# Optimization experiments

Measured on AMD Instinct MI355X. Metric: run time of the kernel, lower is better.

## Reference

```python
import jax, jax.numpy as jnp
import numpy as np

K = 20  # number of unrolled recurrent steps


def setup_inputs() -> dict:
    key = jax.random.key(0)
    k_w, k_b, k0, k1, kv = jax.random.split(key, 5)
    B, d, h = 4096, 128, 256
    w = jax.random.normal(k_w, (B, d, d), dtype=jnp.float32) * 0.05
    b = jax.random.normal(k_b, (B, d), dtype=jnp.float32)
    W0 = jax.random.normal(k0, (h, 2 * d), dtype=jnp.float32) * 0.05
    W1 = jax.random.normal(k1, (h, h), dtype=jnp.float32) * 0.05
    V = jax.random.normal(kv, (d, h), dtype=jnp.float32) * 0.05
    return {"w": w, "b": b, "W0": W0, "W1": W1, "V": V}


def _cell(x, w, b, W0, W1, V):
    # gradient = w @ x - b  -> [B, d]
    grad = jnp.einsum('bij,bj->bi', w, x) - b
    h = jnp.concatenate([-grad, x], axis=-1)      # [B, 2d]
    h = jax.nn.relu(h @ W0.T)                     # [B, h0]
    h = jax.nn.relu(h @ W1.T)                     # [B, h1]
    return h @ V.T                                # [B, d]


def reference(w, b, W0, W1, V):
    x0 = jnp.zeros_like(b)

    def step(x, _):
        return _cell(x, w, b, W0, W1, V), None

    x, _ = jax.lax.scan(step, x0, None, length=K)
    return x
```

## Files before the change

### kernel.cpp

```cpp
#include <hip/hip_runtime.h>
#include <stdint.h>

#define KSTEPS 20
#define EPB 4
#define NBLOCKS 1024
#define NTHREADS 512

#define WQ_E_STRIDE 33792
#define FB_STRIDE   1056
#define WQ_OFF      0
#define HB_OFF      135168
#define H0B_OFF     137344
#define H1B_OFF     139520
#define SMEM_BYTES  141696

#define ACT_STRIDE 544

typedef short bf16x8 __attribute__((ext_vector_type(8)));
typedef float f32x4  __attribute__((ext_vector_type(4)));

static __device__ __forceinline__ uint32_t f2bf(float x) {
    union { float f; uint32_t u; } v; v.f = x;
    return (v.u + 0x7fffu + ((v.u >> 16) & 1u)) >> 16;
}
static __device__ __forceinline__ uint32_t packbf2(float a, float b) {
    uint32_t r;
    asm("v_cvt_pk_bf16_f32 %0, %1, %2" : "=v"(r) : "v"(a), "v"(b));
    return r;
}

__global__ void prep_kernel(const float* __restrict__ W0, const float* __restrict__ W1,
                            const float* __restrict__ V, uint16_t* __restrict__ out)
{
    int i = blockIdx.x * 256 + threadIdx.x;
    float v;
    if (i < 65536) {
        int c = i >> 11, rest = i & 2047, r = rest >> 3, m = rest & 7;
        v = W0[r * 256 + c * 8 + m];
    } else if (i < 131072) {
        int j = i - 65536;
        int c = j >> 11, rest = j & 2047, r = rest >> 3, m = rest & 7;
        v = W1[r * 256 + c * 8 + m];
    } else {
        int j = i - 131072;
        int c = j >> 10, rest = j & 1023, r = rest >> 3, m = rest & 7;
        v = V[r * 256 + c * 8 + m];
    }
    out[i] = (uint16_t)f2bf(v);
}

__global__
__attribute__((amdgpu_flat_work_group_size(512, 512), amdgpu_waves_per_eu(2, 2)))
void mlprnn_main(
    const float* __restrict__ w, const float* __restrict__ b,
    const uint16_t* __restrict__ wp, float* __restrict__ out)
{
    extern __shared__ char smem[];

    const int t  = threadIdx.x;
    const int e0 = blockIdx.x * EPB;

    const int l = t & 63, wv = t >> 6;
    const int row15 = l & 15;
    const int kg    = l >> 4;
    const int cm    = l & 3;
    const bool cok  = row15 < 4;
    const int mt0 = 2 * wv, mt1 = 2 * wv + 1;

    const int e_g  = wv >> 1;
    const int mh   = wv & 1;

    const bf16x8* w0v = (const bf16x8*)wp;
    const bf16x8* w1v = w0v + 32 * 256;
    const bf16x8* vv  = w1v + 32 * 256;

    bf16x8 a0w[8], a1w[8], b0w[8], b1w[8], vw[8];
    #pragma unroll
    for (int kk = 0; kk < 8; ++kk) {
        a0w[kk] = w0v[(kk * 4 + kg) * 256 + mt0 * 16 + row15];
        a1w[kk] = w0v[(kk * 4 + kg) * 256 + mt1 * 16 + row15];
        b0w[kk] = w1v[(kk * 4 + kg) * 256 + mt0 * 16 + row15];
        b1w[kk] = w1v[(kk * 4 + kg) * 256 + mt1 * 16 + row15];
        vw[kk]  = vv[(kk * 4 + kg) * 128 + wv * 16 + row15];
    }
    f32x4 bseed[4];
    #pragma unroll
    for (int mt = 0; mt < 4; ++mt)
        bseed[mt] = *(const f32x4*)(b + (size_t)(e0 + e_g) * 128 + mh * 64 + mt * 16 + kg * 4);

    {
        int e = t >> 7, feat = t & 127;
        float bv = b[(size_t)(e0 + e) * 128 + feat];
        *(uint16_t*)(smem + HB_OFF + e * ACT_STRIDE + feat * 2) = (uint16_t)f2bf(bv);
        *(uint16_t*)(smem + HB_OFF + e * ACT_STRIDE + 256 + feat * 2) = 0;
    }
    __syncthreads();

    #define STAGE_CHUNK(C) do {                                                   \
        const float4* wg_ = (const float4*)w;                                     \
        _Pragma("unroll")                                                         \
        for (int it = (C) * 8; it < (C) * 8 + 8; ++it) {                          \
            int g  = it * NTHREADS + t;                                           \
            int e  = g >> 12;                                                     \
            int gg = g & 4095;                                                    \
            int r  = gg >> 5, q = gg & 31;                                        \
            float4 f = wg_[(size_t)(e0 + e) * 4096 + gg];                         \
            uint2 pk = { packbf2(-f.x, -f.y), packbf2(-f.z, -f.w) };              \
            int kt_s = q >> 3, kg_s = (q >> 1) & 3, h = q & 1;                    \
            int fb   = (r >> 4) * 4 + kt_s;                                       \
            int byte = e * WQ_E_STRIDE + fb * FB_STRIDE                           \
                     + (kg_s * 16 + (r & 15)) * 16 + h * 8;                       \
            *(uint2*)(smem + WQ_OFF + byte) = pk;                                 \
        }                                                                         \
    } while (0)

    const char* wqA = smem + WQ_OFF + e_g * WQ_E_STRIDE + l * 16;
    const char* xB  = smem + HB_OFF + e_g * ACT_STRIDE + 256 + kg * 16;

    const char* hbB = smem + HB_OFF  + cm * ACT_STRIDE + kg * 16;
    const char* h0B = smem + H0B_OFF + cm * ACT_STRIDE + kg * 16;
    const char* h1B = smem + H1B_OFF + cm * ACT_STRIDE + kg * 16;

    bf16x8 gw0h[4], gw1h[4];

    #define PHASE_GRAD() do {                                                     \
        bf16x8 bx[4];                                                             \
        _Pragma("unroll")                                                         \
        for (int kt = 0; kt < 4; ++kt) bx[kt] = *(const bf16x8*)(xB + kt * 64);   \
        f32x4 ag0 = bseed[0], ag1 = bseed[1], ag2 = bseed[2], ag3 = bseed[3];     \
        _Pragma("unroll")                                                         \
        for (int kt = 0; kt < 4; ++kt) {                                          \
            bf16x8 a2 = *(const bf16x8*)(wqA + (((mh * 4 + 2) * 4 + kt) * FB_STRIDE)); \
            bf16x8 a3 = *(const bf16x8*)(wqA + (((mh * 4 + 3) * 4 + kt) * FB_STRIDE)); \
            ag0 = __builtin_amdgcn_mfma_f32_16x16x32_bf16(gw0h[kt], bx[kt], ag0, 0, 0, 0); \
            ag1 = __builtin_amdgcn_mfma_f32_16x16x32_bf16(gw1h[kt], bx[kt], ag1, 0, 0, 0); \
            ag2 = __builtin_amdgcn_mfma_f32_16x16x32_bf16(a2, bx[kt], ag2, 0, 0, 0); \
            ag3 = __builtin_amdgcn_mfma_f32_16x16x32_bf16(a3, bx[kt], ag3, 0, 0, 0); \
        }                                                                         \
        char* gw = smem + HB_OFF + e_g * ACT_STRIDE;                              \
        if (row15 == 0) *(uint2*)(gw + (mh * 64 + 0 * 16 + kg * 4) * 2)           \
            = (uint2){ packbf2(ag0[0], ag0[1]), packbf2(ag0[2], ag0[3]) };        \
        if (row15 == 1) *(uint2*)(gw + (mh * 64 + 1 * 16 + kg * 4) * 2)           \
            = (uint2){ packbf2(ag1[0], ag1[1]), packbf2(ag1[2], ag1[3]) };        \
        if (row15 == 2) *(uint2*)(gw + (mh * 64 + 2 * 16 + kg * 4) * 2)           \
            = (uint2){ packbf2(ag2[0], ag2[1]), packbf2(ag2[2], ag2[3]) };        \
        if (row15 == 3) *(uint2*)(gw + (mh * 64 + 3 * 16 + kg * 4) * 2)           \
            = (uint2){ packbf2(ag3[0], ag3[1]), packbf2(ag3[2], ag3[3]) };        \
    } while (0)

    #define PHASE_MLP(SRC, AW0, AW1, DST) do {                                    \
        f32x4 acc0 = {0.f, 0.f, 0.f, 0.f}, acc0b = {0.f, 0.f, 0.f, 0.f};          \
        f32x4 acc1 = {0.f, 0.f, 0.f, 0.f}, acc1b = {0.f, 0.f, 0.f, 0.f};          \
        _Pragma("unroll")                                                         \
        for (int kk = 0; kk < 4; ++kk) {                                          \
            bf16x8 bf = *(const bf16x8*)((SRC) + kk * 64);                        \
            acc0 = __builtin_amdgcn_mfma_f32_16x16x32_bf16(AW0[kk], bf, acc0, 0, 0, 0); \
            acc1 = __builtin_amdgcn_mfma_f32_16x16x32_bf16(AW1[kk], bf, acc1, 0, 0, 0); \
        }                                                                         \
        _Pragma("unroll")                                                         \
        for (int kk = 4; kk < 8; ++kk) {                                          \
            bf16x8 bf = *(const bf16x8*)((SRC) + kk * 64);                        \
            acc0b = __builtin_amdgcn_mfma_f32_16x16x32_bf16(AW0[kk], bf, acc0b, 0, 0, 0); \
            acc1b = __builtin_amdgcn_mfma_f32_16x16x32_bf16(AW1[kk], bf, acc1b, 0, 0, 0); \
        }                                                                         \
        acc0 += acc0b; acc1 += acc1b;                                             \
        if (cok) {                                                                \
            uint2 q0 = { packbf2(fmaxf(acc0[0], 0.f), fmaxf(acc0[1], 0.f)),       \
                         packbf2(fmaxf(acc0[2], 0.f), fmaxf(acc0[3], 0.f)) };     \
            uint2 q1 = { packbf2(fmaxf(acc1[0], 0.f), fmaxf(acc1[1], 0.f)),       \
                         packbf2(fmaxf(acc1[2], 0.f), fmaxf(acc1[3], 0.f)) };     \
            *(uint2*)(smem + (DST) + row15 * ACT_STRIDE + (mt0 * 16 + kg * 4) * 2) = q0; \
            *(uint2*)(smem + (DST) + row15 * ACT_STRIDE + (mt1 * 16 + kg * 4) * 2) = q1; \
        }                                                                         \
    } while (0)

    #define PHASE_V(K) do {                                                       \
        f32x4 acc = {0.f, 0.f, 0.f, 0.f}, accb = {0.f, 0.f, 0.f, 0.f};            \
        _Pragma("unroll")                                                         \
        for (int kk = 0; kk < 4; ++kk) {                                          \
            bf16x8 bf = *(const bf16x8*)(h1B + kk * 64);                          \
            acc = __builtin_amdgcn_mfma_f32_16x16x32_bf16(vw[kk], bf, acc, 0, 0, 0); \
        }                                                                         \
        _Pragma("unroll")                                                         \
        for (int kk = 4; kk < 8; ++kk) {                                          \
            bf16x8 bf = *(const bf16x8*)(h1B + kk * 64);                          \
            accb = __builtin_amdgcn_mfma_f32_16x16x32_bf16(vw[kk], bf, accb, 0, 0, 0); \
        }                                                                         \
        acc += accb;                                                              \
        if (cok) {                                                                \
            const int r = wv * 16 + kg * 4;                                       \
            uint2 q = { packbf2(acc[0], acc[1]), packbf2(acc[2], acc[3]) };       \
            *(uint2*)(smem + HB_OFF + row15 * ACT_STRIDE + 256 + r * 2) = q;      \
            if ((K) == KSTEPS - 1) {                                              \
                *(f32x4*)(&out[(size_t)(e0 + row15) * 128 + r]) = acc;            \
            }                                                                     \
        }                                                                         \
    } while (0)

    STAGE_CHUNK(0);
    PHASE_MLP(hbB, a0w, a1w, H0B_OFF); __syncthreads();
    STAGE_CHUNK(1);
    PHASE_MLP(h0B, b0w, b1w, H1B_OFF); __syncthreads();
    STAGE_CHUNK(2);
    PHASE_V(0); __syncthreads();
    STAGE_CHUNK(3);
    __syncthreads();

    #pragma unroll
    for (int kt = 0; kt < 4; ++kt) {
        gw0h[kt] = *(const bf16x8*)(wqA + (((mh * 4 + 0) * 4 + kt) * FB_STRIDE));
        gw1h[kt] = *(const bf16x8*)(wqA + (((mh * 4 + 1) * 4 + kt) * FB_STRIDE));
    }

    #pragma unroll 1
    for (int k = 1; k < KSTEPS; ++k) {
        PHASE_GRAD(); __syncthreads();
        PHASE_MLP(hbB, a0w, a1w, H0B_OFF); __syncthreads();
        PHASE_MLP(h0B, b0w, b1w, H1B_OFF); __syncthreads();
        PHASE_V(k); __syncthreads();
    }
}

extern "C" void kernel_launch(void* const* d_in, const int* in_sizes, int n_in,
                              void* d_out, int out_size, void* d_ws, size_t ws_size,
                              hipStream_t stream)
{
    const float* w  = (const float*)d_in[0];
    const float* b  = (const float*)d_in[1];
    const float* W0 = (const float*)d_in[2];
    const float* W1 = (const float*)d_in[3];
    const float* V  = (const float*)d_in[4];
    float* out = (float*)d_out;
    uint16_t* wp = (uint16_t*)d_ws;

    prep_kernel<<<640, 256, 0, stream>>>(W0, W1, V, wp);

    hipFuncSetAttribute((const void*)mlprnn_main,
                        hipFuncAttributeMaxDynamicSharedMemorySize, SMEM_BYTES);
    mlprnn_main<<<NBLOCKS, NTHREADS, SMEM_BYTES, stream>>>(w, b, wp, out);
}
```

Baseline: 179.0 us.

## Overlap x-half of first MLP layer with gradient phase

The first MLP layer's contribution from the x half of the concatenated input is now computed during the gradient phase, since x is already available then. After the barrier, only the gradient half (first four k-tiles) remains, and it is added to the precomputed partial. This shortens the serial dependency chain between the gradient and first-layer phases and interleaves independent MFMAs. The cost is extra accumulator registers live across the barrier, which could raise register pressure.

Measured after the change: 212.7 us. 1.19x slower.

```diff
diff --git a/kernel.cpp b/kernel.cpp
--- a/kernel.cpp
+++ b/kernel.cpp
@@ -123,31 +123,6 @@
 
     bf16x8 gw0h[4], gw1h[4];
 
-    #define PHASE_GRAD() do {                                                     \
-        bf16x8 bx[4];                                                             \
-        _Pragma("unroll")                                                         \
-        for (int kt = 0; kt < 4; ++kt) bx[kt] = *(const bf16x8*)(xB + kt * 64);   \
-        f32x4 ag0 = bseed[0], ag1 = bseed[1], ag2 = bseed[2], ag3 = bseed[3];     \
-        _Pragma("unroll")                                                         \
-        for (int kt = 0; kt < 4; ++kt) {                                          \
-            bf16x8 a2 = *(const bf16x8*)(wqA + (((mh * 4 + 2) * 4 + kt) * FB_STRIDE)); \
-            bf16x8 a3 = *(const bf16x8*)(wqA + (((mh * 4 + 3) * 4 + kt) * FB_STRIDE)); \
-            ag0 = __builtin_amdgcn_mfma_f32_16x16x32_bf16(gw0h[kt], bx[kt], ag0, 0, 0, 0); \
-            ag1 = __builtin_amdgcn_mfma_f32_16x16x32_bf16(gw1h[kt], bx[kt], ag1, 0, 0, 0); \
-            ag2 = __builtin_amdgcn_mfma_f32_16x16x32_bf16(a2, bx[kt], ag2, 0, 0, 0); \
-            ag3 = __builtin_amdgcn_mfma_f32_16x16x32_bf16(a3, bx[kt], ag3, 0, 0, 0); \
-        }                                                                         \
-        char* gw = smem + HB_OFF + e_g * ACT_STRIDE;                              \
-        if (row15 == 0) *(uint2*)(gw + (mh * 64 + 0 * 16 + kg * 4) * 2)           \
-            = (uint2){ packbf2(ag0[0], ag0[1]), packbf2(ag0[2], ag0[3]) };        \
-        if (row15 == 1) *(uint2*)(gw + (mh * 64 + 1 * 16 + kg * 4) * 2)           \
-            = (uint2){ packbf2(ag1[0], ag1[1]), packbf2(ag1[2], ag1[3]) };        \
-        if (row15 == 2) *(uint2*)(gw + (mh * 64 + 2 * 16 + kg * 4) * 2)           \
-            = (uint2){ packbf2(ag2[0], ag2[1]), packbf2(ag2[2], ag2[3]) };        \
-        if (row15 == 3) *(uint2*)(gw + (mh * 64 + 3 * 16 + kg * 4) * 2)           \
-            = (uint2){ packbf2(ag3[0], ag3[1]), packbf2(ag3[2], ag3[3]) };        \
-    } while (0)
-
     #define PHASE_MLP(SRC, AW0, AW1, DST) do {                                    \
         f32x4 acc0 = {0.f, 0.f, 0.f, 0.f}, acc0b = {0.f, 0.f, 0.f, 0.f};          \
         f32x4 acc1 = {0.f, 0.f, 0.f, 0.f}, acc1b = {0.f, 0.f, 0.f, 0.f};          \
@@ -214,8 +189,58 @@
 
     #pragma unroll 1
     for (int k = 1; k < KSTEPS; ++k) {
-        PHASE_GRAD(); __syncthreads();
-        PHASE_MLP(hbB, a0w, a1w, H0B_OFF); __syncthreads();
+        f32x4 px0 = {0.f, 0.f, 0.f, 0.f};
+        f32x4 px1 = {0.f, 0.f, 0.f, 0.f};
+        {
+            bf16x8 bx[4];
+            #pragma unroll
+            for (int kt = 0; kt < 4; ++kt) bx[kt] = *(const bf16x8*)(xB + kt * 64);
+            f32x4 ag0 = bseed[0], ag1 = bseed[1], ag2 = bseed[2], ag3 = bseed[3];
+            #pragma unroll
+            for (int kt = 0; kt < 4; ++kt) {
+                bf16x8 a2 = *(const bf16x8*)(wqA + (((mh * 4 + 2) * 4 + kt) * FB_STRIDE));
+                bf16x8 a3 = *(const bf16x8*)(wqA + (((mh * 4 + 3) * 4 + kt) * FB_STRIDE));
+                bf16x8 bh = *(const bf16x8*)(hbB + (4 + kt) * 64);
+                ag0 = __builtin_amdgcn_mfma_f32_16x16x32_bf16(gw0h[kt], bx[kt], ag0, 0, 0, 0);
+                ag1 = __builtin_amdgcn_mfma_f32_16x16x32_bf16(gw1h[kt], bx[kt], ag1, 0, 0, 0);
+                ag2 = __builtin_amdgcn_mfma_f32_16x16x32_bf16(a2, bx[kt], ag2, 0, 0, 0);
+                ag3 = __builtin_amdgcn_mfma_f32_16x16x32_bf16(a3, bx[kt], ag3, 0, 0, 0);
+                px0 = __builtin_amdgcn_mfma_f32_16x16x32_bf16(a0w[4 + kt], bh, px0, 0, 0, 0);
+                px1 = __builtin_amdgcn_mfma_f32_16x16x32_bf16(a1w[4 + kt], bh, px1, 0, 0, 0);
+            }
+            char* gw = smem + HB_OFF + e_g * ACT_STRIDE;
+            if (row15 == 0) *(uint2*)(gw + (mh * 64 + 0 * 16 + kg * 4) * 2)
+                = (uint2){ packbf2(ag0[0], ag0[1]), packbf2(ag0[2], ag0[3]) };
+            if (row15 == 1) *(uint2*)(gw + (mh * 64 + 1 * 16 + kg * 4) * 2)
+                = (uint2){ packbf2(ag1[0], ag1[1]), packbf2(ag1[2], ag1[3]) };
+            if (row15 == 2) *(uint2*)(gw + (mh * 64 + 2 * 16 + kg * 4) * 2)
+                = (uint2){ packbf2(ag2[0], ag2[1]), packbf2(ag2[2], ag2[3]) };
+            if (row15 == 3) *(uint2*)(gw + (mh * 64 + 3 * 16 + kg * 4) * 2)
+                = (uint2){ packbf2(ag3[0], ag3[1]), packbf2(ag3[2], ag3[3]) };
+        }
+        __syncthreads();
+
+        {
+            f32x4 acc0 = {0.f, 0.f, 0.f, 0.f};
+            f32x4 acc1 = {0.f, 0.f, 0.f, 0.f};
+            #pragma unroll
+            for (int kk = 0; kk < 4; ++kk) {
+                bf16x8 bf = *(const bf16x8*)(hbB + kk * 64);
+                acc0 = __builtin_amdgcn_mfma_f32_16x16x32_bf16(a0w[kk], bf, acc0, 0, 0, 0);
+                acc1 = __builtin_amdgcn_mfma_f32_16x16x32_bf16(a1w[kk], bf, acc1, 0, 0, 0);
+            }
+            acc0 += px0; acc1 += px1;
+            if (cok) {
+                uint2 q0 = { packbf2(fmaxf(acc0[0], 0.f), fmaxf(acc0[1], 0.f)),
+                             packbf2(fmaxf(acc0[2], 0.f), fmaxf(acc0[3], 0.f)) };
+                uint2 q1 = { packbf2(fmaxf(acc1[0], 0.f), fmaxf(acc1[1], 0.f)),
+                             packbf2(fmaxf(acc1[2], 0.f), fmaxf(acc1[3], 0.f)) };
+                *(uint2*)(smem + H0B_OFF + row15 * ACT_STRIDE + (mt0 * 16 + kg * 4) * 2) = q0;
+                *(uint2*)(smem + H0B_OFF + row15 * ACT_STRIDE + (mt1 * 16 + kg * 4) * 2) = q1;
+            }
+        }
+        __syncthreads();
+
         PHASE_MLP(h0B, b0w, b1w, H1B_OFF); __syncthreads();
         PHASE_V(k); __syncthreads();
     }
```
